# Kernel optimization log

Hardware: AMD Instinct MI355X
Metric: run time of the kernel (lower is better)

Reference implementation:

```python
import jax, jax.numpy as jnp
import numpy as np

DIM = 64
IN_CH = 3 * DIM          # 192
HID_CH = 2 * IN_CH       # 384
BN_EPS = 1e-5


def setup_inputs() -> dict:
    key = jax.random.key(0)
    ks = jax.random.split(key, 6)
    B, H, W = 8, 256, 256
    x = jax.random.normal(ks[0], (B, H, W, DIM), dtype=jnp.float32)
    gamma = jnp.ones((IN_CH,), dtype=jnp.float32)
    beta = jnp.zeros((IN_CH,), dtype=jnp.float32)
    w_in = jax.random.normal(ks[1], (HID_CH, IN_CH), dtype=jnp.float32) * (1.0 / np.sqrt(IN_CH))
    w_dw = jax.random.normal(ks[2], (HID_CH, 1, 3, 3), dtype=jnp.float32) * (1.0 / 3.0)
    w_out = jax.random.normal(ks[3], (IN_CH, HID_CH), dtype=jnp.float32) * (1.0 / np.sqrt(HID_CH))
    res_scale = jnp.ones((1,), dtype=jnp.float32)
    return {"x": x, "gamma": gamma, "beta": beta, "w_in": w_in,
            "w_dw": w_dw, "w_out": w_out, "res_scale": res_scale}


def _dwt(xc):
    # xc: (B, C, H, W) NCHW, H and W even. Haar via strided slices.
    B, C, H, W = xc.shape
    a = xc[:, :, 0::2, 0::2]
    b = xc[:, :, 0::2, 1::2]
    c = xc[:, :, 1::2, 0::2]
    d = xc[:, :, 1::2, 1::2]
    LLc = (a + b + c + d) * 0.5
    LHc = (a - b + c - d) * 0.5
    HLc = (a + b - c - d) * 0.5
    HHc = (a - b - c + d) * 0.5
    # torch grouped conv output channel order is (channel, subband) flattened,
    # then chunk(4) splits contiguously -> each chunk mixes subbands. Replicate.
    y = jnp.stack([LLc, LHc, HLc, HHc], axis=2)        # (B, C, 4, h, w)
    y = y.reshape(B, 4 * C, H // 2, W // 2)
    return y[:, 0*C:1*C], y[:, 1*C:2*C], y[:, 2*C:3*C], y[:, 3*C:4*C]


def _iwt(LL, LH, HL, HH):
    B, C, h, w = LL.shape
    # cat along channels then view(B,4,C,h,w): interprets as (4, C) layout.
    x4 = jnp.concatenate([LL, LH, HL, HH], axis=1).reshape(B, 4, C, h, w)
    # out[b,c,2p+r,2q+s] = x4[b, 2r+s, c, p, q]
    arr = x4.transpose(0, 2, 1, 3, 4).reshape(B, C, 2, 2, h, w)
    out = arr.transpose(0, 1, 4, 2, 5, 3).reshape(B, C, 2 * h, 2 * w)
    return out


def _mlp(high, gamma, beta, w_in, w_dw, w_out, res_scale):
    # BatchNorm2d in training mode: biased batch stats over (B, H, W)
    mean = jnp.mean(high, axis=(0, 2, 3))
    var = jnp.var(high, axis=(0, 2, 3))
    xn = (high - mean[None, :, None, None]) * jax.lax.rsqrt(var + BN_EPS)[None, :, None, None]
    xn = xn * gamma[None, :, None, None] + beta[None, :, None, None]
    h = jnp.einsum('oc,bchw->bohw', w_in, xn)           # 1x1 conv, no bias
    h = jax.lax.conv_general_dilated(
        h, w_dw, window_strides=(1, 1), padding=((1, 1), (1, 1)),
        dimension_numbers=('NCHW', 'OIHW', 'NCHW'),
        feature_group_count=HID_CH)                      # depthwise 3x3
    h = jax.nn.gelu(h, approximate=False)                # torch nn.GELU default: exact erf
    h = jnp.einsum('oc,bchw->bohw', w_out, h)            # 1x1 conv, no bias
    return high + res_scale[0] * h


def reference(x, gamma, beta, w_in, w_dw, w_out, res_scale):
    xc = jnp.transpose(x, (0, 3, 1, 2))                  # NHWC -> NCHW
    LL, LH, HL, HH = _dwt(xc)
    high = jnp.concatenate([LH, HL, HH], axis=1)         # (B, 3C, h, w)
    high_enh = _mlp(high, gamma, beta, w_in, w_dw, w_out, res_scale)
    C = LL.shape[1]
    LHo, HLo, HHo = high_enh[:, :C], high_enh[:, C:2*C], high_enh[:, 2*C:]
    out = _iwt(LL, LHo, HLo, HHo)                        # (B, C, H, W)
    return jnp.transpose(out, (0, 2, 3, 1))              # back to NHWC
```

## Files before the change

kernel.cpp:

```cpp
#include <hip/hip_runtime.h>
#include <math.h>

typedef unsigned short u16;
typedef unsigned int u32;
typedef __attribute__((ext_vector_type(4))) float f4;
typedef __attribute__((ext_vector_type(2))) float f2;
typedef __attribute__((ext_vector_type(4))) u16 u16x4;
typedef __attribute__((ext_vector_type(8))) u16 u16x8;
typedef __attribute__((ext_vector_type(8))) short bf8;

#define N_IMG 8
#define HS 128
#define NPOS (N_IMG*HS*HS)
#define IN_CH 192
#define HID_CH 384

__device__ __forceinline__ u16 f2bf(float f) {
  union { float f; u32 u; } v; v.f = f;
  u32 r = v.u + 0x7FFFu + ((v.u >> 16) & 1u);
  return (u16)(r >> 16);
}
__device__ __forceinline__ float bf2f(u16 u) {
  union { u32 u; float f; } v; v.u = ((u32)u) << 16; return v.f;
}
__device__ __forceinline__ f2 bfpair(u32 d) {
  union { u32 u; float f; } lo, hi;
  lo.u = d << 16; hi.u = d & 0xffff0000u;
  f2 r; r[0] = lo.f; r[1] = hi.f; return r;
}
__device__ __forceinline__ float gelu_fast(float x) {
  float x2 = x * x;
  float z = x * (-2.302208f - 0.102942f * x2);
  float e = __builtin_amdgcn_exp2f(z);
  return x * __builtin_amdgcn_rcpf(1.0f + e);
}
__device__ __forceinline__ void gl_lds16(const u16* g, u16* l) {
  __builtin_amdgcn_global_load_lds(
      (__attribute__((address_space(1))) void*)(u16*)g,
      (__attribute__((address_space(3))) void*)l, 16, 0, 0);
}

__global__ void k0_zero(float* stats) { stats[threadIdx.x] = 0.0f; }

__global__ __launch_bounds__(256) void k1_dwt(
    const float* __restrict__ x,
    u16* __restrict__ high,
    float* __restrict__ out,
    float* __restrict__ stats)
{
  const int blk = blockIdx.x;
  const int b = blk >> 8, i = (blk >> 1) & 127, jh = blk & 1;
  const int t = threadIdx.x;
  const int c4 = t & 15;
  const int j0 = t >> 4;
  const int jbase = jh * 64 + j0;
  const int rowE = ((b * 256 + 2 * i) * 256) * 64;
  const int rowO = rowE + 256 * 64;
  const bool isHigh = (c4 >= 4);

  float sacc[16], qacc[16];
#pragma unroll
  for (int v = 0; v < 16; v++) { sacc[v] = 0.f; qacc[v] = 0.f; }

  f4 R[2][4];
  {
    const int colE = (2 * jbase) * 64 + c4 * 4;
    R[0][0] = *(const f4*)(x + rowE + colE);
    R[0][1] = *(const f4*)(x + rowE + colE + 64);
    R[0][2] = *(const f4*)(x + rowO + colE);
    R[0][3] = *(const f4*)(x + rowO + colE + 64);
  }

#pragma unroll
  for (int iter = 0; iter < 4; ++iter) {
    const int cur = iter & 1, nxt = cur ^ 1;
    if (iter < 3) {
      const int jn = jbase + 16 * (iter + 1);
      const int colE = (2 * jn) * 64 + c4 * 4;
      R[nxt][0] = *(const f4*)(x + rowE + colE);
      R[nxt][1] = *(const f4*)(x + rowE + colE + 64);
      R[nxt][2] = *(const f4*)(x + rowO + colE);
      R[nxt][3] = *(const f4*)(x + rowO + colE + 64);
    }
    const int j = jbase + 16 * iter;
    f4 va = R[cur][0], vb = R[cur][1], vc = R[cur][2], vd = R[cur][3];
    f4 sb0 = (va + vb + vc + vd) * 0.5f;
    f4 sb1 = (va - vb + vc - vd) * 0.5f;
    f4 sb2 = (va + vb - vc - vd) * 0.5f;
    f4 sb3 = (va - vb - vc + vd) * 0.5f;

    if (!isHigh) {
      float* dst = out + rowE + (2 * j) * 64 + 16 * c4;
#pragma unroll
      for (int cc = 0; cc < 4; cc++) {
        f4 ov;
        ov[0] = sb0[cc]; ov[1] = sb1[cc]; ov[2] = sb2[cc]; ov[3] = sb3[cc];
        ((f4*)dst)[cc] = ov;
      }
    } else {
      const int n = b * 16384 + i * 128 + j;
      u16* dst = high + n * 192 + 16 * (c4 - 4);
#pragma unroll
      for (int half = 0; half < 2; half++) {
        u16x8 pk;
#pragma unroll
        for (int cc2 = 0; cc2 < 2; cc2++) {
          const int cc = half * 2 + cc2;
          pk[cc2 * 4 + 0] = f2bf(sb0[cc]);
          pk[cc2 * 4 + 1] = f2bf(sb1[cc]);
          pk[cc2 * 4 + 2] = f2bf(sb2[cc]);
          pk[cc2 * 4 + 3] = f2bf(sb3[cc]);
        }
        *(u16x8*)(dst + half * 8) = pk;
      }
#pragma unroll
      for (int cc = 0; cc < 4; cc++) {
        float e0 = sb0[cc], e1 = sb1[cc], e2 = sb2[cc], e3 = sb3[cc];
        sacc[cc * 4 + 0] += e0; qacc[cc * 4 + 0] += e0 * e0;
        sacc[cc * 4 + 1] += e1; qacc[cc * 4 + 1] += e1 * e1;
        sacc[cc * 4 + 2] += e2; qacc[cc * 4 + 2] += e2 * e2;
        sacc[cc * 4 + 3] += e3; qacc[cc * 4 + 3] += e3 * e3;
      }
    }
  }

  float vals[32];
#pragma unroll
  for (int v = 0; v < 16; v++) { vals[v] = sacc[v]; vals[16 + v] = qacc[v]; }
#pragma unroll
  for (int v = 0; v < 32; v++) {
    float xx = vals[v];
    xx += __shfl_down(xx, 32);
    xx += __shfl_down(xx, 16);
    vals[v] = xx;
  }
  __shared__ float sred[4][12][32];
  const int lane = t & 63, wave = t >> 6;
  if (lane >= 4 && lane < 16) {
#pragma unroll
    for (int v = 0; v < 32; v++) sred[wave][lane - 4][v] = vals[v];
  }
  __syncthreads();
  if (t < 192) {
    const int g = t >> 4, L = t & 15;
    float s = sred[0][g][L] + sred[1][g][L] + sred[2][g][L] + sred[3][g][L];
    float q = sred[0][g][16 + L] + sred[1][g][16 + L] + sred[2][g][16 + L] + sred[3][g][16 + L];
    atomicAdd(&stats[t], s);
    atomicAdd(&stats[192 + t], q);
  }
}

__global__ void k2a(const float* __restrict__ stats, const float* __restrict__ gamma,
                    const float* __restrict__ beta, float* __restrict__ st)
{
  const int t = threadIdx.x;
  if (t < 192) {
    const float inv_n = 1.0f / 131072.0f;
    float mean = stats[t] * inv_n;
    float var = stats[192 + t] * inv_n - mean * mean;
    var = fmaxf(var, 0.0f);
    float s = gamma[t] * rsqrtf(var + 1e-5f);
    st[t] = s;
    st[192 + t] = beta[t] - mean * s;
  }
}

__global__ __launch_bounds__(64) void k2b(
    const float* __restrict__ w_in, const float* __restrict__ w_out,
    const float* __restrict__ st, const float* __restrict__ res_scale,
    const float* __restrict__ wdw,
    u16* __restrict__ w_in_f, float* __restrict__ bias1, u16* __restrict__ w_out_f,
    float* __restrict__ wdw_pk)
{
  const int o = blockIdx.x, lane = threadIdx.x;
  if (o < 384) {
    float p = 0.f;
    for (int c = lane; c < 192; c += 64) {
      float w = w_in[o * 192 + c];
      w_in_f[o * 192 + c] = f2bf(w * st[c]);
      p += w * st[192 + c];
    }
#pragma unroll
    for (int off = 32; off; off >>= 1) p += __shfl_down(p, off);
    if (lane == 0) bias1[o] = p;
  } else if (o < 576) {
    const int o2 = o - 384;
    const float rs = res_scale[0];
    for (int c = lane; c < 384; c += 64)
      w_out_f[o2 * 384 + c] = f2bf(w_out[o2 * 384 + c] * rs);
  } else {
    const int oct = o - 576;
    for (int q = lane; q < 72; q += 64) {
      const int tap = q >> 3, e = q & 7;
      wdw_pk[oct * 72 + q] = wdw[(oct * 8 + e) * 9 + tap];
    }
  }
}

__global__ __launch_bounds__(256) void k3_gemm1(
    const u16* __restrict__ A,
    const u16* __restrict__ Bw,
    const float* __restrict__ bias,
    u16* __restrict__ C,
    int Mg)
{
  __shared__ __align__(16) u16 smem[128 * 136];
  u16* As = smem;
  u16* Bs = smem + 128 * 32;
  const int t = threadIdx.x;
  const int lane = t & 63, wave = t >> 6;
  const int wm = wave >> 1, wn = wave & 1;
  const int m0 = blockIdx.x * 128;
  const int n0 = blockIdx.y * 128;
  const int lrow = lane >> 2, lcol = lane & 3;
  const int frow = lane & 15, fk = (lane >> 4) * 8;

  f4 acc[4][4];
#pragma unroll
  for (int a = 0; a < 4; a++)
#pragma unroll
    for (int b = 0; b < 4; b++) acc[a][b] = 0.0f;

  for (int ks = 0; ks < 6; ++ks) {
    const int kb = ks * 32;
#pragma unroll
    for (int l = 0; l < 2; ++l) {
      const int r = wave * 32 + l * 16 + lrow;
      gl_lds16(A + (size_t)(m0 + r) * 192 + kb + lcol * 8, As + (wave * 32 + l * 16) * 32);
      gl_lds16(Bw + (size_t)(n0 + r) * 192 + kb + lcol * 8, Bs + (wave * 32 + l * 16) * 32);
    }
    __syncthreads();
    bf8 af[4], bfr[4];
#pragma unroll
    for (int fm = 0; fm < 4; ++fm)
      af[fm] = *(const bf8*)(As + (wm * 64 + fm * 16 + frow) * 32 + fk);
#pragma unroll
    for (int fn = 0; fn < 4; ++fn)
      bfr[fn] = *(const bf8*)(Bs + (wn * 64 + fn * 16 + frow) * 32 + fk);
#pragma unroll
    for (int fm = 0; fm < 4; ++fm)
#pragma unroll
      for (int fn = 0; fn < 4; ++fn)
        acc[fm][fn] = __builtin_amdgcn_mfma_f32_16x16x32_bf16(af[fm], bfr[fn], acc[fm][fn], 0, 0, 0);
    __syncthreads();
  }

  u16* Ct = smem;
  const int r0 = (lane >> 4) * 4, cc = lane & 15;
#pragma unroll
  for (int fn = 0; fn < 4; ++fn) {
    const int ncol = wn * 64 + fn * 16 + cc;
    const float bv = bias[n0 + ncol];
#pragma unroll
    for (int fm = 0; fm < 4; ++fm) {
      const int mr = wm * 64 + fm * 16 + r0;
#pragma unroll
      for (int r = 0; r < 4; ++r)
        Ct[(mr + r) * 136 + ncol] = f2bf(acc[fm][fn][r] + bv);
    }
  }
  __syncthreads();
#pragma unroll
  for (int it = 0; it < 8; ++it) {
    const int idx = it * 256 + t;
    const int row = idx >> 4, seg = idx & 15;
    const int col = n0 + seg * 8;
    const int hsel = (col >= 192) ? 1 : 0;
    u16x8 v = *(const u16x8*)(Ct + row * 136 + seg * 8);
    *(u16x8*)(C + (size_t)hsel * Mg * 192 + (size_t)(m0 + row) * 192 + (col - hsel * 192)) = v;
  }
}

__global__ __launch_bounds__(256) void k45_dwgemm2(
    const u16* __restrict__ h1,
    const float* __restrict__ wdw_pk,
    const u16* __restrict__ Bw,
    const u16* __restrict__ high,
    float* __restrict__ out,
    int chunkStart, int Mg)
{
  __shared__ __align__(16) char smem_raw[13824 + 45056];
  float* wlds = (float*)smem_raw;
  u16* h1t = (u16*)(smem_raw + 13824);
  u16* Asl = (u16*)(smem_raw + 13824 + 24576);
  u16* Bs  = (u16*)(smem_raw + 13824 + 24576 + 8192);
  float* Stg = (float*)(smem_raw + 13824);

  const int t = threadIdx.x;
  const int lane = t & 63, wave = t >> 6;
  const int wm = wave >> 1, wn = wave & 1;
  const int nwg = gridDim.x;
  const int wg = (blockIdx.x & 7) * (nwg >> 3) + (blockIdx.x >> 3);
  const int img = wg >> 7, irow = wg & 127;
  const int m0 = wg * 128;
  const int lrow = lane >> 2, lcol = lane & 3;
  const int frow = lane & 15, fk = (lane >> 4) * 8;

  for (int q = t; q < 3456; q += 256) wlds[q] = wdw_pk[q];
  if (irow == 0) {
    for (int q = t; q < 512; q += 256) *(u16x8*)(h1t + q * 8) = (u16x8)(0);
  }
  if (irow == 127) {
    for (int q = t; q < 512; q += 256) *(u16x8*)(h1t + 2 * 4096 + q * 8) = (u16x8)(0);
  }

  f4 acc[4][6];
#pragma unroll
  for (int a = 0; a < 4; a++)
#pragma unroll
    for (int b = 0; b < 6; b++) acc[a][b] = 0.0f;

  const int oct = t & 3, j0q = t >> 2;

  for (int ks = 0; ks < 12; ++ks) {
    const int kb = ks * 32;
    const int half = (ks >= 6) ? 1 : 0;
    const int klocal = kb - half * 192;
    const u16* hsrc = h1 + (size_t)half * Mg * 192 + klocal;

    for (int is = wave; is < 24; is += 4) {
      const int dy = is >> 3, seg = is & 7;
      const int gr = irow - 1 + dy;
      if (gr >= 0 && gr < 128) {
        const int j = seg * 16 + (lane >> 2);
        gl_lds16(hsrc + (size_t)(img * 16384 + gr * 128 + j) * 192 + (lane & 3) * 8,
                 h1t + (dy * 128 + seg * 16) * 32);
      }
    }
#pragma unroll
    for (int l = 0; l < 3; ++l) {
      const int rb = wave * 48 + l * 16 + lrow;
      gl_lds16(Bw + (size_t)rb * 384 + kb + lcol * 8, Bs + (wave * 48 + l * 16) * 32);
    }
    __syncthreads();

    f4 w4[9][2];
    {
      const float* wp = wlds + (ks * 4 + oct) * 72;
#pragma unroll
      for (int tap = 0; tap < 9; ++tap) {
        w4[tap][0] = *(const f4*)(wp + tap * 8);
        w4[tap][1] = *(const f4*)(wp + tap * 8 + 4);
      }
    }
#pragma unroll
    for (int jj2 = 0; jj2 < 2; ++jj2) {
      const int jj = j0q + jj2 * 64;
      f2 accd[4];
#pragma unroll
      for (int p = 0; p < 4; p++) accd[p] = (f2)(0.f);
#pragma unroll
      for (int dy = 0; dy < 3; ++dy) {
        const int base = (dy * 128 + jj) * 32 + oct * 8;
        u16x8 xc = *(const u16x8*)(h1t + base);
        u16x8 xl = (jj != 0)   ? *(const u16x8*)(h1t + base - 32) : (u16x8)(0);
        u16x8 xr = (jj != 127) ? *(const u16x8*)(h1t + base + 32) : (u16x8)(0);
        union { u16x8 v; u32 d[4]; } ul, uc, ur;
        ul.v = xl; uc.v = xc; ur.v = xr;
#pragma unroll
        for (int p = 0; p < 4; p++) {
          f2 wl, wc, wr;
          wl[0] = w4[dy * 3 + 0][p >> 1][2 * (p & 1)];
          wl[1] = w4[dy * 3 + 0][p >> 1][2 * (p & 1) + 1];
          wc[0] = w4[dy * 3 + 1][p >> 1][2 * (p & 1)];
          wc[1] = w4[dy * 3 + 1][p >> 1][2 * (p & 1) + 1];
          wr[0] = w4[dy * 3 + 2][p >> 1][2 * (p & 1)];
          wr[1] = w4[dy * 3 + 2][p >> 1][2 * (p & 1) + 1];
          accd[p] += wl * bfpair(ul.d[p]) + wc * bfpair(uc.d[p]) + wr * bfpair(ur.d[p]);
        }
      }
      u16x8 ov;
#pragma unroll
      for (int p = 0; p < 4; p++) {
        ov[2 * p]     = f2bf(gelu_fast(accd[p][0]));
        ov[2 * p + 1] = f2bf(gelu_fast(accd[p][1]));
      }
      *(u16x8*)(Asl + jj * 32 + oct * 8) = ov;
    }
    __syncthreads();

    bf8 af[4], bfr[6];
#pragma unroll
    for (int fm = 0; fm < 4; ++fm)
      af[fm] = *(const bf8*)(Asl + (wm * 64 + fm * 16 + frow) * 32 + fk);
#pragma unroll
    for (int fn = 0; fn < 6; ++fn)
      bfr[fn] = *(const bf8*)(Bs + (wn * 96 + fn * 16 + frow) * 32 + fk);
#pragma unroll
    for (int fm = 0; fm < 4; ++fm)
#pragma unroll
      for (int fn = 0; fn < 6; ++fn)
        acc[fm][fn] = __builtin_amdgcn_mfma_f32_16x16x32_bf16(af[fm], bfr[fn], acc[fm][fn], 0, 0, 0);
    __syncthreads();
  }

  const int r0 = (lane >> 4) * 4, ccol = lane & 15;
#pragma unroll
  for (int bsel = 0; bsel < 3; ++bsel) {
    if (bsel) __syncthreads();
#pragma unroll
    for (int fn = 0; fn < 6; ++fn) {
      const int oc = wn * 96 + fn * 16 + ccol;
      if ((oc >> 6) == bsel) {
        const int c = oc & 63;
#pragma unroll
        for (int fm = 0; fm < 4; ++fm) {
          const int jb = wm * 64 + fm * 16 + r0;
#pragma unroll
          for (int r = 0; r < 4; ++r)
            Stg[(jb + r) * 68 + c] = acc[fm][fn][r];
        }
      }
    }
    __syncthreads();
    const int p = (bsel + 1) >> 1, q = (bsel + 1) & 1;
#pragma unroll
    for (int it = 0; it < 2; ++it) {
      const int jr = (t >> 2) + it * 64;
      const int cq = (t & 3) * 16;
      const int np = chunkStart + m0 + jr;
      const int bi = np >> 14, rem = np & 16383, ii = rem >> 7;
      const u16* hp = high + (size_t)np * 192 + bsel * 64 + cq;
      union { u16x8 v; u32 d[4]; } h0, h1u;
      h0.v = *(const u16x8*)hp;
      h1u.v = *(const u16x8*)(hp + 8);
      const float* sp = Stg + jr * 68 + cq;
      f4 o0 = *(const f4*)sp;
      f4 o1 = *(const f4*)(sp + 4);
      f4 o2 = *(const f4*)(sp + 8);
      f4 o3 = *(const f4*)(sp + 12);
      f2 a0 = bfpair(h0.d[0]), a1 = bfpair(h0.d[1]), a2 = bfpair(h0.d[2]), a3 = bfpair(h0.d[3]);
      f2 b0 = bfpair(h1u.d[0]), b1 = bfpair(h1u.d[1]), b2 = bfpair(h1u.d[2]), b3 = bfpair(h1u.d[3]);
      o0[0] += a0[0]; o0[1] += a0[1]; o0[2] += a1[0]; o0[3] += a1[1];
      o1[0] += a2[0]; o1[1] += a2[1]; o1[2] += a3[0]; o1[3] += a3[1];
      o2[0] += b0[0]; o2[1] += b0[1]; o2[2] += b1[0]; o2[3] += b1[1];
      o3[0] += b2[0]; o3[1] += b2[1]; o3[2] += b3[0]; o3[3] += b3[1];
      float* op = out + (size_t)(((bi * 256 + 2 * ii + p) * 256) + (2 * jr + q)) * 64 + cq;
      *(f4*)op       = o0;
      *(f4*)(op + 4) = o1;
      *(f4*)(op + 8) = o2;
      *(f4*)(op + 12)= o3;
    }
  }
}

extern "C" void kernel_launch(void* const* d_in, const int* in_sizes, int n_in,
                              void* d_out, int out_size, void* d_ws, size_t ws_size,
                              hipStream_t stream)
{
  const float* x        = (const float*)d_in[0];
  const float* gamma    = (const float*)d_in[1];
  const float* beta     = (const float*)d_in[2];
  const float* w_in     = (const float*)d_in[3];
  const float* w_dw     = (const float*)d_in[4];
  const float* w_out    = (const float*)d_in[5];
  const float* res_scale= (const float*)d_in[6];
  float* out = (float*)d_out;
  char* ws = (char*)d_ws;

  float* stats   = (float*)ws;
  float* st      = (float*)(ws + 2048);
  float* bias1   = (float*)(ws + 4096);
  u16*   w_in_f  = (u16*)(ws + 8192);
  u16*   w_out_f = (u16*)(ws + 8192 + 147456);
  float* wdw_pk  = (float*)(ws + 8192 + 2 * 147456);
  u16*   high    = (u16*)(ws + (size_t)(1 << 19));
  const size_t off_h1 = (size_t)(1 << 19) + (size_t)NPOS * 192 * 2;
  const size_t imgBytes = (size_t)16384 * 384 * 2;
  int G = 8;
  while (G > 1 && off_h1 + (size_t)G * imgBytes > ws_size) G >>= 1;
  u16* h1 = (u16*)(ws + off_h1);

  k0_zero<<<1, 384, 0, stream>>>(stats);
  k1_dwt<<<2048, 256, 0, stream>>>(x, high, out, stats);
  k2a<<<1, 256, 0, stream>>>(stats, gamma, beta, st);
  k2b<<<624, 64, 0, stream>>>(w_in, w_out, st, res_scale, w_dw, w_in_f, bias1, w_out_f, wdw_pk);

  for (int cs = 0; cs < 8; cs += G) {
    const int chunkStart = cs * 16384;
    const int Mg = G * 16384;
    k3_gemm1<<<dim3(Mg / 128, 3), 256, 0, stream>>>(high + (size_t)chunkStart * 192, w_in_f, bias1, h1, Mg);
    k45_dwgemm2<<<G * 128, 256, 0, stream>>>(h1, wdw_pk, w_out_f, high, out, chunkStart, Mg);
  }
}
```

Baseline: 400.3 us.

## Prefetch next K-step h1 tile during MFMA and read dw weights from global

```diff
diff --git a/kernel.cpp b/kernel.cpp
--- a/kernel.cpp
+++ b/kernel.cpp
@@ -279,12 +279,11 @@
     float* __restrict__ out,
     int chunkStart, int Mg)
 {
-  __shared__ __align__(16) char smem_raw[13824 + 45056];
-  float* wlds = (float*)smem_raw;
-  u16* h1t = (u16*)(smem_raw + 13824);
-  u16* Asl = (u16*)(smem_raw + 13824 + 24576);
-  u16* Bs  = (u16*)(smem_raw + 13824 + 24576 + 8192);
-  float* Stg = (float*)(smem_raw + 13824);
+  __shared__ __align__(16) char smem_raw[45056];
+  u16* h1t = (u16*)smem_raw;
+  u16* Asl = (u16*)(smem_raw + 24576);
+  u16* Bs  = (u16*)(smem_raw + 32768);
+  float* Stg = (float*)smem_raw;
 
   const int t = threadIdx.x;
   const int lane = t & 63, wave = t >> 6;
@@ -295,8 +294,8 @@
   const int m0 = wg * 128;
   const int lrow = lane >> 2, lcol = lane & 3;
   const int frow = lane & 15, fk = (lane >> 4) * 8;
-
-  for (int q = t; q < 3456; q += 256) wlds[q] = wdw_pk[q];
+  const int oct = t & 3, j0q = t >> 2;
+
   if (irow == 0) {
     for (int q = t; q < 512; q += 256) *(u16x8*)(h1t + q * 8) = (u16x8)(0);
   }
@@ -310,33 +309,40 @@
 #pragma unroll
     for (int b = 0; b < 6; b++) acc[a][b] = 0.0f;
 
-  const int oct = t & 3, j0q = t >> 2;
+#define STAGE_H1T(KS)                                                            \
+  {                                                                              \
+    const int half_ = ((KS) >= 6) ? 1 : 0;                                       \
+    const u16* hsrc_ = h1 + (size_t)half_ * Mg * 192 + ((KS) * 32 - half_ * 192);\
+    for (int is = wave; is < 24; is += 4) {                                      \
+      const int dy = is >> 3, seg = is & 7;                                      \
+      const int gr = irow - 1 + dy;                                              \
+      if (gr >= 0 && gr < 128) {                                                 \
+        const int j = seg * 16 + (lane >> 2);                                    \
+        gl_lds16(hsrc_ + (size_t)(img * 16384 + gr * 128 + j) * 192 + (lane & 3) * 8, \
+                 h1t + (dy * 128 + seg * 16) * 32);                              \
+      }                                                                          \
+    }                                                                            \
+  }
+
+#define STAGE_BS(KS)                                                             \
+  {                                                                              \
+    const int kb_ = (KS) * 32;                                                   \
+    _Pragma("unroll")                                                            \
+    for (int l = 0; l < 3; ++l) {                                                \
+      const int rb = wave * 48 + l * 16 + lrow;                                  \
+      gl_lds16(Bw + (size_t)rb * 384 + kb_ + lcol * 8, Bs + (wave * 48 + l * 16) * 32); \
+    }                                                                            \
+  }
+
+  STAGE_H1T(0);
+  STAGE_BS(0);
 
   for (int ks = 0; ks < 12; ++ks) {
-    const int kb = ks * 32;
-    const int half = (ks >= 6) ? 1 : 0;
-    const int klocal = kb - half * 192;
-    const u16* hsrc = h1 + (size_t)half * Mg * 192 + klocal;
-
-    for (int is = wave; is < 24; is += 4) {
-      const int dy = is >> 3, seg = is & 7;
-      const int gr = irow - 1 + dy;
-      if (gr >= 0 && gr < 128) {
-        const int j = seg * 16 + (lane >> 2);
-        gl_lds16(hsrc + (size_t)(img * 16384 + gr * 128 + j) * 192 + (lane & 3) * 8,
-                 h1t + (dy * 128 + seg * 16) * 32);
-      }
-    }
-#pragma unroll
-    for (int l = 0; l < 3; ++l) {
-      const int rb = wave * 48 + l * 16 + lrow;
-      gl_lds16(Bw + (size_t)rb * 384 + kb + lcol * 8, Bs + (wave * 48 + l * 16) * 32);
-    }
     __syncthreads();
 
     f4 w4[9][2];
     {
-      const float* wp = wlds + (ks * 4 + oct) * 72;
+      const float* wp = wdw_pk + (ks * 4 + oct) * 72;
 #pragma unroll
       for (int tap = 0; tap < 9; ++tap) {
         w4[tap][0] = *(const f4*)(wp + tap * 8);
@@ -379,6 +385,8 @@
     }
     __syncthreads();
 
+    if (ks < 11) STAGE_H1T(ks + 1);
+
     bf8 af[4], bfr[6];
 #pragma unroll
     for (int fm = 0; fm < 4; ++fm)
@@ -392,7 +400,11 @@
       for (int fn = 0; fn < 6; ++fn)
         acc[fm][fn] = __builtin_amdgcn_mfma_f32_16x16x32_bf16(af[fm], bfr[fn], acc[fm][fn], 0, 0, 0);
     __syncthreads();
-  }
+
+    if (ks < 11) STAGE_BS(ks + 1);
+  }
+#undef STAGE_H1T
+#undef STAGE_BS
 
   const int r0 = (lane >> 4) * 4, ccol = lane & 15;
 #pragma unroll
```

Result: slower. 473.1 us (+18.2%).

## Process two image rows per workgroup in fused depthwise+GEMM2 kernel

Applied to the files above, without the earlier changes.

```diff
diff --git a/kernel.cpp b/kernel.cpp
--- a/kernel.cpp
+++ b/kernel.cpp
@@ -210,8 +210,8 @@
   const int t = threadIdx.x;
   const int lane = t & 63, wave = t >> 6;
   const int wm = wave >> 1, wn = wave & 1;
-  const int m0 = blockIdx.x * 128;
-  const int n0 = blockIdx.y * 128;
+  const int m0 = (blockIdx.x / 3) * 128;
+  const int n0 = (blockIdx.x % 3) * 128;
   const int lrow = lane >> 2, lcol = lane & 3;
   const int frow = lane & 15, fk = (lane >> 4) * 8;
 
@@ -271,7 +271,7 @@
   }
 }
 
-__global__ __launch_bounds__(256) void k45_dwgemm2(
+__global__ __launch_bounds__(512) void k45_dwgemm2(
     const u16* __restrict__ h1,
     const float* __restrict__ wdw_pk,
     const u16* __restrict__ Bw,
@@ -279,58 +279,49 @@
     float* __restrict__ out,
     int chunkStart, int Mg)
 {
-  __shared__ __align__(16) char smem_raw[13824 + 45056];
+  __shared__ __align__(16) char smem_raw[75264];
   float* wlds = (float*)smem_raw;
   u16* h1t = (u16*)(smem_raw + 13824);
-  u16* Asl = (u16*)(smem_raw + 13824 + 24576);
-  u16* Bs  = (u16*)(smem_raw + 13824 + 24576 + 8192);
-  float* Stg = (float*)(smem_raw + 13824);
+  u16* Asl = (u16*)(smem_raw + 46592);
+  u16* Bs  = (u16*)(smem_raw + 62976);
+  float* Stg = (float*)smem_raw;
 
   const int t = threadIdx.x;
   const int lane = t & 63, wave = t >> 6;
   const int wm = wave >> 1, wn = wave & 1;
   const int nwg = gridDim.x;
   const int wg = (blockIdx.x & 7) * (nwg >> 3) + (blockIdx.x >> 3);
-  const int img = wg >> 7, irow = wg & 127;
-  const int m0 = wg * 128;
+  const int img = wg >> 6, rp = wg & 63;
+  const int m0 = wg * 256;
   const int lrow = lane >> 2, lcol = lane & 3;
   const int frow = lane & 15, fk = (lane >> 4) * 8;
-
-  for (int q = t; q < 3456; q += 256) wlds[q] = wdw_pk[q];
-  if (irow == 0) {
-    for (int q = t; q < 512; q += 256) *(u16x8*)(h1t + q * 8) = (u16x8)(0);
-  }
-  if (irow == 127) {
-    for (int q = t; q < 512; q += 256) *(u16x8*)(h1t + 2 * 4096 + q * 8) = (u16x8)(0);
-  }
+  const int oct = t & 3, jcol = t >> 2;
+
+  for (int q = t; q < 3456; q += 512) wlds[q] = wdw_pk[q];
+  if (rp == 0)  *(u16x8*)(h1t + t * 8) = (u16x8)(0);
+  if (rp == 63) *(u16x8*)(h1t + 3 * 4096 + t * 8) = (u16x8)(0);
 
   f4 acc[4][6];
 #pragma unroll
   for (int a = 0; a < 4; a++)
 #pragma unroll
     for (int b = 0; b < 6; b++) acc[a][b] = 0.0f;
-
-  const int oct = t & 3, j0q = t >> 2;
 
   for (int ks = 0; ks < 12; ++ks) {
     const int kb = ks * 32;
     const int half = (ks >= 6) ? 1 : 0;
-    const int klocal = kb - half * 192;
-    const u16* hsrc = h1 + (size_t)half * Mg * 192 + klocal;
-
-    for (int is = wave; is < 24; is += 4) {
-      const int dy = is >> 3, seg = is & 7;
-      const int gr = irow - 1 + dy;
+    const u16* hsrc = h1 + (size_t)half * Mg * 192 + (kb - half * 192);
+
+    for (int is = wave; is < 32; is += 8) {
+      const int hr = is >> 3, seg = is & 7;
+      const int gr = 2 * rp - 1 + hr;
       if (gr >= 0 && gr < 128) {
-        const int j = seg * 16 + (lane >> 2);
-        gl_lds16(hsrc + (size_t)(img * 16384 + gr * 128 + j) * 192 + (lane & 3) * 8,
-                 h1t + (dy * 128 + seg * 16) * 32);
-      }
-    }
-#pragma unroll
-    for (int l = 0; l < 3; ++l) {
-      const int rb = wave * 48 + l * 16 + lrow;
-      gl_lds16(Bw + (size_t)rb * 384 + kb + lcol * 8, Bs + (wave * 48 + l * 16) * 32);
+        gl_lds16(hsrc + (size_t)(img * 16384 + gr * 128 + seg * 16 + (lane >> 2)) * 192 + (lane & 3) * 8,
+                 h1t + (hr * 128 + seg * 16) * 32);
+      }
+    }
+    for (int is = wave; is < 12; is += 8) {
+      gl_lds16(Bw + (size_t)(is * 16 + lrow) * 384 + kb + lcol * 8, Bs + is * 16 * 32);
     }
     __syncthreads();
 
@@ -343,40 +334,55 @@
         w4[tap][1] = *(const f4*)(wp + tap * 8 + 4);
       }
     }
-#pragma unroll
-    for (int jj2 = 0; jj2 < 2; ++jj2) {
-      const int jj = j0q + jj2 * 64;
-      f2 accd[4];
-#pragma unroll
-      for (int p = 0; p < 4; p++) accd[p] = (f2)(0.f);
-#pragma unroll
-      for (int dy = 0; dy < 3; ++dy) {
-        const int base = (dy * 128 + jj) * 32 + oct * 8;
-        u16x8 xc = *(const u16x8*)(h1t + base);
-        u16x8 xl = (jj != 0)   ? *(const u16x8*)(h1t + base - 32) : (u16x8)(0);
-        u16x8 xr = (jj != 127) ? *(const u16x8*)(h1t + base + 32) : (u16x8)(0);
-        union { u16x8 v; u32 d[4]; } ul, uc, ur;
-        ul.v = xl; uc.v = xc; ur.v = xr;
+    f2 acc0[4], acc1[4];
+#pragma unroll
+    for (int p = 0; p < 4; p++) { acc0[p] = (f2)(0.f); acc1[p] = (f2)(0.f); }
+
+#pragma unroll
+    for (int hr = 0; hr < 4; ++hr) {
+      const int base = (hr * 128 + jcol) * 32 + oct * 8;
+      u16x8 xc = *(const u16x8*)(h1t + base);
+      u16x8 xl = (jcol != 0)   ? *(const u16x8*)(h1t + base - 32) : (u16x8)(0);
+      u16x8 xr = (jcol != 127) ? *(const u16x8*)(h1t + base + 32) : (u16x8)(0);
+      union { u16x8 v; u32 d[4]; } ul, uc, ur;
+      ul.v = xl; uc.v = xc; ur.v = xr;
+      f2 xm[4], x0[4], xp[4];
+#pragma unroll
+      for (int p = 0; p < 4; p++) {
+        xm[p] = bfpair(ul.d[p]); x0[p] = bfpair(uc.d[p]); xp[p] = bfpair(ur.d[p]);
+      }
+      if (hr < 3) {
 #pragma unroll
         for (int p = 0; p < 4; p++) {
           f2 wl, wc, wr;
-          wl[0] = w4[dy * 3 + 0][p >> 1][2 * (p & 1)];
-          wl[1] = w4[dy * 3 + 0][p >> 1][2 * (p & 1) + 1];
-          wc[0] = w4[dy * 3 + 1][p >> 1][2 * (p & 1)];
-          wc[1] = w4[dy * 3 + 1][p >> 1][2 * (p & 1) + 1];
-          wr[0] = w4[dy * 3 + 2][p >> 1][2 * (p & 1)];
-          wr[1] = w4[dy * 3 + 2][p >> 1][2 * (p & 1) + 1];
-          accd[p] += wl * bfpair(ul.d[p]) + wc * bfpair(uc.d[p]) + wr * bfpair(ur.d[p]);
+          wl[0] = w4[hr * 3 + 0][p >> 1][2 * (p & 1)]; wl[1] = w4[hr * 3 + 0][p >> 1][2 * (p & 1) + 1];
+          wc[0] = w4[hr * 3 + 1][p >> 1][2 * (p & 1)]; wc[1] = w4[hr * 3 + 1][p >> 1][2 * (p & 1) + 1];
+          wr[0] = w4[hr * 3 + 2][p >> 1][2 * (p & 1)]; wr[1] = w4[hr * 3 + 2][p >> 1][2 * (p & 1) + 1];
+          acc0[p] += wl * xm[p] + wc * x0[p] + wr * xp[p];
         }
       }
-      u16x8 ov;
-#pragma unroll
-      for (int p = 0; p < 4; p++) {
-        ov[2 * p]     = f2bf(gelu_fast(accd[p][0]));
-        ov[2 * p + 1] = f2bf(gelu_fast(accd[p][1]));
-      }
-      *(u16x8*)(Asl + jj * 32 + oct * 8) = ov;
-    }
+      if (hr > 0) {
+        const int dy = hr - 1;
+#pragma unroll
+        for (int p = 0; p < 4; p++) {
+          f2 wl, wc, wr;
+          wl[0] = w4[dy * 3 + 0][p >> 1][2 * (p & 1)]; wl[1] = w4[dy * 3 + 0][p >> 1][2 * (p & 1) + 1];
+          wc[0] = w4[dy * 3 + 1][p >> 1][2 * (p & 1)]; wc[1] = w4[dy * 3 + 1][p >> 1][2 * (p & 1) + 1];
+          wr[0] = w4[dy * 3 + 2][p >> 1][2 * (p & 1)]; wr[1] = w4[dy * 3 + 2][p >> 1][2 * (p & 1) + 1];
+          acc1[p] += wl * xm[p] + wc * x0[p] + wr * xp[p];
+        }
+      }
+    }
+    u16x8 ov0, ov1;
+#pragma unroll
+    for (int p = 0; p < 4; p++) {
+      ov0[2 * p]     = f2bf(gelu_fast(acc0[p][0]));
+      ov0[2 * p + 1] = f2bf(gelu_fast(acc0[p][1]));
+      ov1[2 * p]     = f2bf(gelu_fast(acc1[p][0]));
+      ov1[2 * p + 1] = f2bf(gelu_fast(acc1[p][1]));
+    }
+    *(u16x8*)(Asl + jcol * 32 + oct * 8) = ov0;
+    *(u16x8*)(Asl + (128 + jcol) * 32 + oct * 8) = ov1;
     __syncthreads();
 
     bf8 af[4], bfr[6];
@@ -416,10 +422,10 @@
     const int p = (bsel + 1) >> 1, q = (bsel + 1) & 1;
 #pragma unroll
     for (int it = 0; it < 2; ++it) {
-      const int jr = (t >> 2) + it * 64;
+      const int jr = (t >> 2) + it * 128;
       const int cq = (t & 3) * 16;
       const int np = chunkStart + m0 + jr;
-      const int bi = np >> 14, rem = np & 16383, ii = rem >> 7;
+      const int bi = np >> 14, rem = np & 16383, ii = rem >> 7, jj = rem & 127;
       const u16* hp = high + (size_t)np * 192 + bsel * 64 + cq;
       union { u16x8 v; u32 d[4]; } h0, h1u;
       h0.v = *(const u16x8*)hp;
@@ -435,7 +441,7 @@
       o1[0] += a2[0]; o1[1] += a2[1]; o1[2] += a3[0]; o1[3] += a3[1];
       o2[0] += b0[0]; o2[1] += b0[1]; o2[2] += b1[0]; o2[3] += b1[1];
       o3[0] += b2[0]; o3[1] += b2[1]; o3[2] += b3[0]; o3[3] += b3[1];
-      float* op = out + (size_t)(((bi * 256 + 2 * ii + p) * 256) + (2 * jr + q)) * 64 + cq;
+      float* op = out + (size_t)(((bi * 256 + 2 * ii + p) * 256) + (2 * jj + q)) * 64 + cq;
       *(f4*)op       = o0;
       *(f4*)(op + 4) = o1;
       *(f4*)(op + 8) = o2;
@@ -479,7 +485,7 @@
   for (int cs = 0; cs < 8; cs += G) {
     const int chunkStart = cs * 16384;
     const int Mg = G * 16384;
-    k3_gemm1<<<dim3(Mg / 128, 3), 256, 0, stream>>>(high + (size_t)chunkStart * 192, w_in_f, bias1, h1, Mg);
-    k45_dwgemm2<<<G * 128, 256, 0, stream>>>(h1, wdw_pk, w_out_f, high, out, chunkStart, Mg);
-  }
-}
+    k3_gemm1<<<3 * (Mg / 128), 256, 0, stream>>>(high + (size_t)chunkStart * 192, w_in_f, bias1, h1, Mg);
+    k45_dwgemm2<<<G * 64, 512, 0, stream>>>(h1, wdw_pk, w_out_f, high, out, chunkStart, Mg);
+  }
+}
```

After: 414.3 us. +3.5%, slower.
